# Kernel optimization log

Hardware: AMD Instinct MI355X
Metric: run time of the kernel (lower is better)

The kernel has to match this reference:

```python
import jax, jax.numpy as jnp
import numpy as np
from jax import lax

EPS = 1e-8

def _cosine_cost(x, y):
    # 1 - cosine_similarity over feature dim: [B,N,M]
    xn = x / jnp.clip(jnp.linalg.norm(x, axis=-1, keepdims=True), EPS)
    yn = y / jnp.clip(jnp.linalg.norm(y, axis=-1, keepdims=True), EPS)
    return 1.0 - jnp.einsum('bnd,bmd->bnm', xn, yn)

def _dtw_table(cost):
    # cost: [B,N,M] -> cumulative cost tc: [B,N,M]
    # tc[i,j] = cost[i,j] + min(tc[i-1,j-1], tc[i-1,j], tc[i,j-1])
    B, N, M = cost.shape
    row0 = jnp.cumsum(cost[:, 0, :], axis=1)  # [B,M]

    def col_step(left, inp):
        c, pdiag, pup = inp  # each [B]
        v = c + jnp.minimum(jnp.minimum(pdiag, pup), left)
        return v, v

    def row_step(prev, cost_row):
        # prev, cost_row: [B,M]
        first = prev[:, 0] + cost_row[:, 0]  # [B]
        xs = (cost_row[:, 1:].T, prev[:, :-1].T, prev[:, 1:].T)  # [M-1,B]
        _, rest = lax.scan(col_step, first, xs)  # [M-1,B]
        row = jnp.concatenate([first[:, None], rest.T], axis=1)  # [B,M]
        return row, row

    _, rows = lax.scan(row_step, row0, jnp.swapaxes(cost[:, 1:, :], 0, 1))
    tc = jnp.concatenate([row0[:, None, :], jnp.swapaxes(rows, 0, 1)], axis=1)
    return tc

def _backtrack(tc):
    # tc: [N,M] -> 0/1 path matrix [N,M]; tie-break diag > up > left,
    # matching the torch equality-chain order.
    N, M = tc.shape
    path0 = jnp.zeros((N, M), tc.dtype).at[N - 1, M - 1].set(1.0)

    def cond(s):
        i, j, _ = s
        return jnp.logical_and(i > 0, j > 0)

    def body(s):
        i, j, p = s
        a = tc[i - 1, j - 1]
        b = tc[i - 1, j]
        c = tc[i, j - 1]
        diag = jnp.logical_and(a <= b, a <= c)
        up = jnp.logical_and(jnp.logical_not(diag), b <= c)
        ni = jnp.where(jnp.logical_or(diag, up), i - 1, i)
        nj = jnp.where(jnp.logical_or(diag, jnp.logical_not(up)), j - 1, j)
        p = p.at[ni, nj].set(1.0)
        return ni, nj, p

    _, _, p = lax.while_loop(cond, body, (jnp.int32(N - 1), jnp.int32(M - 1), path0))
    return p.at[0, 0].set(1.0)

def setup_inputs() -> dict:
    key = jax.random.key(0)
    kx, ky = jax.random.split(key)
    B, N, M, D = 64, 512, 512, 256
    x = jax.random.normal(kx, (B, N, D), dtype=jnp.float32)
    y = jax.random.normal(ky, (B, M, D), dtype=jnp.float32)
    return {"x": x, "y": y}

def reference(x, y):
    cost = _cosine_cost(x, y)                 # [B,N,M]
    tc = _dtw_table(cost)                     # [B,N,M]
    path = jax.vmap(_backtrack)(tc)           # [B,N,M]
    pos = jax.nn.logsumexp(jnp.sum(cost * path, axis=1), axis=1)  # [B]
    neg = jax.nn.logsumexp(jnp.sum(cost, axis=1), axis=1)         # [B]
    return pos - neg
```

## Files before the change

kernel.cpp:

```cpp
#include <hip/hip_runtime.h>
#include <hip/hip_bf16.h>
#include <stdint.h>

typedef __attribute__((ext_vector_type(8))) short short8v;
typedef __attribute__((ext_vector_type(4))) float float4v;
typedef __attribute__((ext_vector_type(4))) unsigned short ushort4v;
typedef __attribute__((ext_vector_type(4))) unsigned int uint4v;

#define FINF __builtin_huge_valf()
#define BB 64
#define NN 512
#define DD 256
#define TT_SKEW 640


static __device__ __forceinline__ unsigned short f2bf(float f) {
  union { float f; uint32_t u; } a; a.f = f;
  uint32_t r = a.u + 0x7fffu + ((a.u >> 16) & 1u);
  return (unsigned short)(r >> 16);
}
static __device__ __forceinline__ float bf2f(uint16_t v) {
  return __uint_as_float(((uint32_t)v) << 16);
}

__global__ __launch_bounds__(64) void pad_zero_kernel(uint16_t* __restrict__ skew)
{
  const int tau = blockIdx.x, b = blockIdx.y, g = threadIdx.x;
  const int r = tau - 2 * g;
  if (r < 0 || r > 511) {
    uint16_t* p = skew + ((size_t)b * TT_SKEW + tau) * NN + g * 8;
    *(uint4v*)p = (uint4v){0u, 0u, 0u, 0u};
  }
}

__global__ __launch_bounds__(256) void norm_cast_kernel(
    const float* __restrict__ x, const float* __restrict__ y,
    uint16_t* __restrict__ xnb, uint16_t* __restrict__ ynb)
{
  const int wave = threadIdx.x >> 6, lane = threadIdx.x & 63;
  const int row = blockIdx.x * 4 + wave;
  const float* src; uint16_t* dst;
  if (row < BB * NN) { src = x + (size_t)row * DD;            dst = xnb + (size_t)row * DD; }
  else               { src = y + (size_t)(row - BB*NN) * DD;  dst = ynb + (size_t)(row - BB*NN) * DD; }
  const float4v v = *(const float4v*)(src + lane * 4);
  float s = v[0]*v[0] + v[1]*v[1] + v[2]*v[2] + v[3]*v[3];
  #pragma unroll
  for (int d = 1; d < 64; d <<= 1) s += __shfl_xor(s, d, 64);
  const float inv = 1.0f / fmaxf(sqrtf(s), 1e-8f);
  ushort4v o;
  o[0] = f2bf(v[0] * inv); o[1] = f2bf(v[1] * inv);
  o[2] = f2bf(v[2] * inv); o[3] = f2bf(v[3] * inv);
  *(ushort4v*)(dst + lane * 4) = o;
}

__global__ __launch_bounds__(256) void gemm_cost_kernel(
    const uint16_t* __restrict__ xnb, const uint16_t* __restrict__ ynb,
    uint16_t* __restrict__ skew)
{
  __shared__ uint16_t As[128 * 32];
  __shared__ uint16_t Bs[128 * 32];
  const int bid = blockIdx.x;
  const int b = bid >> 4, tm = (bid >> 2) & 3, tn = bid & 3;
  const int tid = threadIdx.x, wave = tid >> 6, lane = tid & 63;
  const int wr = wave >> 1, wc = wave & 1;

  const char* Ab = (const char*)(xnb + (size_t)b * NN * DD + (size_t)tm * 128 * DD);
  const char* Bb = (const char*)(ynb + (size_t)b * NN * DD + (size_t)tn * 128 * DD);

  float4v acc[4][4];
  #pragma unroll
  for (int i = 0; i < 4; i++)
    #pragma unroll
    for (int j = 0; j < 4; j++) acc[i][j] = (float4v){0.f, 0.f, 0.f, 0.f};

  const int seg0 = wave * 2;
  const int o0 = seg0 * 1024 + lane * 16;
  const int o1 = o0 + 1024;
  const int r0 = o0 >> 6, c0 = o0 & 63;
  const int r1 = o1 >> 6, c1 = o1 & 63;

  for (int kk = 0; kk < 8; kk++) {
    const int kb = kk * 64;
    __builtin_amdgcn_global_load_lds(
        (const __attribute__((address_space(1))) uint32_t*)(Ab + (size_t)r0 * 512 + kb + c0),
        (__attribute__((address_space(3))) uint32_t*)((char*)As + seg0 * 1024), 16, 0, 0);
    __builtin_amdgcn_global_load_lds(
        (const __attribute__((address_space(1))) uint32_t*)(Ab + (size_t)r1 * 512 + kb + c1),
        (__attribute__((address_space(3))) uint32_t*)((char*)As + (seg0 + 1) * 1024), 16, 0, 0);
    __builtin_amdgcn_global_load_lds(
        (const __attribute__((address_space(1))) uint32_t*)(Bb + (size_t)r0 * 512 + kb + c0),
        (__attribute__((address_space(3))) uint32_t*)((char*)Bs + seg0 * 1024), 16, 0, 0);
    __builtin_amdgcn_global_load_lds(
        (const __attribute__((address_space(1))) uint32_t*)(Bb + (size_t)r1 * 512 + kb + c1),
        (__attribute__((address_space(3))) uint32_t*)((char*)Bs + (seg0 + 1) * 1024), 16, 0, 0);
    __syncthreads();

    short8v af[4], bfr[4];
    #pragma unroll
    for (int mi = 0; mi < 4; mi++) {
      const int rr = wr * 64 + mi * 16 + (lane & 15);
      af[mi] = *(const short8v*)((const char*)As + rr * 64 + (lane >> 4) * 16);
    }
    #pragma unroll
    for (int nj = 0; nj < 4; nj++) {
      const int rr = wc * 64 + nj * 16 + (lane & 15);
      bfr[nj] = *(const short8v*)((const char*)Bs + rr * 64 + (lane >> 4) * 16);
    }
    #pragma unroll
    for (int mi = 0; mi < 4; mi++)
      #pragma unroll
      for (int nj = 0; nj < 4; nj++)
        acc[mi][nj] = __builtin_amdgcn_mfma_f32_16x16x32_bf16(af[mi], bfr[nj], acc[mi][nj], 0, 0, 0);
    __syncthreads();
  }

  uint16_t* Cb = skew + (size_t)b * TT_SKEW * NN;
  #pragma unroll
  for (int mi = 0; mi < 4; mi++)
    #pragma unroll
    for (int nj = 0; nj < 4; nj++) {
      const int cc = tn * 128 + wc * 64 + nj * 16 + (lane & 15);
      const int lg = cc >> 3;
      #pragma unroll
      for (int v = 0; v < 4; v++) {
        const int rr = tm * 128 + wr * 64 + mi * 16 + (lane >> 4) * 4 + v;
        Cb[(size_t)(rr + 2 * lg) * NN + cc] = f2bf(1.0f - acc[mi][nj][v]);
      }
    }
}

__global__ __launch_bounds__(256) void neg_lse_kernel(
    const uint16_t* __restrict__ skew, float* __restrict__ negbuf)
{
  __shared__ float sm[8];
  const int b = blockIdx.x, tid = threadIdx.x;
  const int wave = tid >> 6, lane = tid & 63;
  const uint32_t* p = (const uint32_t*)(skew + (size_t)b * TT_SKEW * NN) + tid;
  float s0 = 0.f, s1 = 0.f;
  #pragma unroll 8
  for (int t = 0; t < TT_SKEW; ++t) {
    const uint32_t w = p[t * 256];
    s0 += __uint_as_float(w << 16);
    s1 += __uint_as_float(w & 0xFFFF0000u);
  }
  float m = fmaxf(s0, s1);
  #pragma unroll
  for (int d = 1; d < 64; d <<= 1) m = fmaxf(m, __shfl_xor(m, d, 64));
  if (lane == 0) sm[wave] = m;
  __syncthreads();
  m = fmaxf(fmaxf(sm[0], sm[1]), fmaxf(sm[2], sm[3]));
  float e = expf(s0 - m) + expf(s1 - m);
  #pragma unroll
  for (int d = 1; d < 64; d <<= 1) e += __shfl_xor(e, d, 64);
  if (lane == 0) sm[4 + wave] = e;
  __syncthreads();
  if (tid == 0) negbuf[b] = m + logf(sm[4] + sm[5] + sm[6] + sm[7]);
}

__global__ __launch_bounds__(64, 1) void dtw_fwd_kernel(
    const uint16_t* __restrict__ skew, uint32_t* __restrict__ decg)
{
  extern __shared__ char lds_raw[];
  const int l = threadIdx.x;
  const int b = blockIdx.x;
  const uint16_t* csk = skew + (size_t)b * TT_SKEW * NN;
  const uint64_t base = (uint64_t)(uintptr_t)csk;
  const bool is0 = (l == 0);
  const uint32_t voff_base = 16u * (uint32_t)l;

  uint4v ringA[8], ringB[8];
  #pragma unroll
  for (int i = 0; i < 8; ++i) {
    const uint32_t voA = voff_base + ((uint32_t)(2 * i) << 10);
    const uint32_t voB = voA + 1024u;
    asm volatile("global_load_dwordx4 %0, %1, %2" : "=v"(ringA[i]) : "v"(voA), "s"(base));
    asm volatile("global_load_dwordx4 %0, %1, %2" : "=v"(ringB[i]) : "v"(voB), "s"(base));
  }

  float tp[8];
  #pragma unroll
  for (int c = 0; c < 8; ++c) tp[c] = FINF;
  float cl0 = FINF, cl1 = FINF, carry = FINF;
  const uint32_t dump_addr = 65536u + (((uint32_t)l) << 2);

  for (int t0 = 0; t0 < 320; t0 += 8) {
    #pragma unroll
    for (int u = 0; u < 8; ++u) {
      const int t = t0 + u;
      float shA = __shfl_up(cl0, 1, 64);
      float shB = __shfl_up(cl1, 1, 64);
      if (is0) { shA = (t == 0) ? 0.0f : FINF; shB = FINF; }
      const float sh_p0 = carry;
      carry = shB;

      asm volatile("s_waitcnt vmcnt(14)" : "+v"(ringA[u]), "+v"(ringB[u]));
      const uint4v A = ringA[u];
      const uint4v Bv = ringB[u];

      const uint32_t rlane = (uint32_t)(t - l);
      const bool valid = rlane < 256u;

      float ca[8], cbv[8], S0[8], S1[8];
      #pragma unroll
      for (int k = 0; k < 4; ++k) {
        ca[2*k]   = __uint_as_float(A[k] << 16);
        ca[2*k+1] = __uint_as_float(A[k] & 0xFFFF0000u);
        cbv[2*k]   = __uint_as_float(Bv[k] << 16);
        cbv[2*k+1] = __uint_as_float(Bv[k] & 0xFFFF0000u);
      }
      S0[0] = ca[0]; S1[0] = cbv[0];
      #pragma unroll
      for (int c = 1; c < 8; ++c) { S0[c] = S0[c-1] + ca[c]; S1[c] = S1[c-1] + cbv[c]; }

      float dcp0[8], mu0[8], w0[8], PW0[8], tn0[8];
      dcp0[0] = sh_p0;
      #pragma unroll
      for (int c = 1; c < 8; ++c) dcp0[c] = tp[c-1];
      #pragma unroll
      for (int c = 0; c < 8; ++c) mu0[c] = fminf(dcp0[c], tp[c]);
      w0[0] = mu0[0];
      #pragma unroll
      for (int c = 1; c < 8; ++c) w0[c] = mu0[c] - S0[c-1];
      PW0[0] = w0[0];
      #pragma unroll
      for (int c = 1; c < 8; ++c) PW0[c] = fminf(PW0[c-1], w0[c]);
      #pragma unroll
      for (int c = 0; c < 8; ++c) tn0[c] = fminf(PW0[c], shA) + S0[c];

      float dcp1[8], mu1[8], w1[8], PW1[8], tn1[8];
      dcp1[0] = shA;
      #pragma unroll
      for (int c = 1; c < 8; ++c) dcp1[c] = tn0[c-1];
      #pragma unroll
      for (int c = 0; c < 8; ++c) mu1[c] = fminf(dcp1[c], tn0[c]);
      w1[0] = mu1[0];
      #pragma unroll
      for (int c = 1; c < 8; ++c) w1[c] = mu1[c] - S1[c-1];
      PW1[0] = w1[0];
      #pragma unroll
      for (int c = 1; c < 8; ++c) PW1[c] = fminf(PW1[c-1], w1[c]);
      #pragma unroll
      for (int c = 0; c < 8; ++c) tn1[c] = fminf(PW1[c], shB) + S1[c];

      uint32_t word = 0;
      {
        float lc0[8], lc1[8];
        lc0[0] = shA; lc1[0] = shB;
        #pragma unroll
        for (int c = 1; c < 8; ++c) { lc0[c] = tn0[c-1]; lc1[c] = tn1[c-1]; }
        #pragma unroll
        for (int c = 0; c < 8; ++c) {
          const uint32_t e0 = (tp[c] < dcp0[c]) ? 1u : 0u;
          const uint32_t d0 = (lc0[c] < mu0[c]) ? 2u : e0;
          const uint32_t e1 = (tn0[c] < dcp1[c]) ? 1u : 0u;
          const uint32_t d1 = (lc1[c] < mu1[c]) ? 2u : e1;
          word |= (d0 << (2 * c)) | (d1 << (16 + 2 * c));
        }
      }
      const uint32_t waddr = valid ? ((rlane << 8) | (((uint32_t)l) << 2)) : dump_addr;
      *(uint32_t*)(lds_raw + waddr) = word;

      #pragma unroll
      for (int c = 0; c < 8; ++c) tp[c] = valid ? tn1[c] : tp[c];
      cl0 = valid ? tn0[7] : cl0;
      cl1 = tp[7];

      {
        int rr = 2 * (t + 8); if (rr > 638) rr = 638;
        const uint32_t voA = voff_base + ((uint32_t)rr << 10);
        const uint32_t voB = voA + 1024u;
        asm volatile("global_load_dwordx4 %0, %1, %2" : "=v"(ringA[u]) : "v"(voA), "s"(base));
        asm volatile("global_load_dwordx4 %0, %1, %2" : "=v"(ringB[u]) : "v"(voB), "s"(base));
      }
    }
  }
  asm volatile("s_waitcnt vmcnt(0)" ::: "memory");

  uint32_t* dg = decg + (size_t)b * 16384;
  #pragma unroll 4
  for (int i = 0; i < 64; ++i)
    *(uint4v*)(dg + i * 256 + l * 4) = *(const uint4v*)(lds_raw + i * 1024 + l * 16);
}

__global__ __launch_bounds__(64, 1) void dtw_bt_kernel(
    const uint16_t* __restrict__ skew, const uint32_t* __restrict__ decg,
    const float* __restrict__ negbuf, float* __restrict__ out)
{
  extern __shared__ char lds_raw[];
  uint16_t* rlo    = (uint16_t*)(lds_raw + 65536);
  uint16_t* rhi    = (uint16_t*)(lds_raw + 66560);
  float*    colpos = (float*)  (lds_raw + 67584);
  const uint32_t* dec32 = (const uint32_t*)lds_raw;

  const int l = threadIdx.x;
  const int b = blockIdx.x;
  const uint16_t* csk = skew + (size_t)b * TT_SKEW * NN;
  const uint32_t* dg = decg + (size_t)b * 16384;

  #pragma unroll 4
  for (int i = 0; i < 64; ++i)
    *(uint4v*)(lds_raw + i * 1024 + l * 16) = *(const uint4v*)(dg + i * 256 + l * 4);
  for (int r = l; r < NN; r += 64) { rlo[r] = 1; rhi[r] = 0; colpos[r] = 0.0f; }
  __syncthreads();

  if (l == 0) {
    int i = NN - 1, j = NN - 1, hicur = NN - 1;
    int cidx = -1; uint32_t cw = 0;
    while (i > 0 && j > 0) {
      const int widx = (i >> 1) * 64 + (j >> 3);
      if (widx != cidx) { cw = dec32[widx]; cidx = widx; }
      const uint32_t dd = (cw >> (((i & 1) << 4) + ((j & 7) << 1))) & 3u;
      if (dd == 2u) { j--; }
      else {
        rlo[i] = (uint16_t)j; rhi[i] = (uint16_t)hicur;
        i--;
        if (dd == 0u) j--;
        hicur = j;
      }
    }
    rlo[i] = (uint16_t)j; rhi[i] = (uint16_t)hicur;
  }
  __syncthreads();
  for (int r = l; r < NN; r += 64) {
    const int lo = rlo[r], hi = rhi[r];
    for (int j = lo; j <= hi; j++) {
      const float cv = bf2f(csk[(size_t)(r + 2 * (j >> 3)) * NN + j]);
      atomicAdd(&colpos[j], cv);
    }
  }
  if (l == 0 && rlo[0] != 0) atomicAdd(&colpos[0], bf2f(csk[0]));
  __syncthreads();

  float mv[8];
  float mx2 = -FINF;
  #pragma unroll
  for (int k = 0; k < 8; k++) { mv[k] = colpos[l + 64 * k]; mx2 = fmaxf(mx2, mv[k]); }
  #pragma unroll
  for (int d = 1; d < 64; d <<= 1) mx2 = fmaxf(mx2, __shfl_xor(mx2, d, 64));
  float se2 = 0.f;
  #pragma unroll
  for (int k = 0; k < 8; k++) se2 += expf(mv[k] - mx2);
  #pragma unroll
  for (int d = 1; d < 64; d <<= 1) se2 += __shfl_xor(se2, d, 64);
  const float pos = mx2 + logf(se2);

  if (l == 0) out[b] = pos - negbuf[b];
}

extern "C" void kernel_launch(void* const* d_in, const int* in_sizes, int n_in,
                              void* d_out, int out_size, void* d_ws, size_t ws_size,
                              hipStream_t stream)
{
  (void)in_sizes; (void)n_in; (void)out_size; (void)ws_size;
  const float* x = (const float*)d_in[0];
  const float* y = (const float*)d_in[1];
  float* out = (float*)d_out;
  char* ws = (char*)d_ws;
  uint16_t* xnb  = (uint16_t*)ws;
  uint16_t* ynb  = (uint16_t*)(ws + (size_t)16777216);
  uint16_t* skew = (uint16_t*)(ws + (size_t)33554432);
  float*  negbuf = (float*)  (ws + (size_t)75497472);
  uint32_t* decg = (uint32_t*)(ws + (size_t)75501568);

  (void)hipFuncSetAttribute((const void*)dtw_fwd_kernel,
                            hipFuncAttributeMaxDynamicSharedMemorySize, 65792);
  (void)hipFuncSetAttribute((const void*)dtw_bt_kernel,
                            hipFuncAttributeMaxDynamicSharedMemorySize, 69632);

  pad_zero_kernel<<<dim3(TT_SKEW, BB), 64, 0, stream>>>(skew);
  norm_cast_kernel<<<16384, 256, 0, stream>>>(x, y, xnb, ynb);
  gemm_cost_kernel<<<1024, 256, 0, stream>>>(xnb, ynb, skew);
  neg_lse_kernel<<<64, 256, 0, stream>>>(skew, negbuf);
  dtw_fwd_kernel<<<64, 64, 65792, stream>>>(skew, decg);
  dtw_bt_kernel<<<64, 64, 69632, stream>>>(skew, decg, negbuf, out);
}
```

Baseline: 297.9 us.

## Interleave two batches per wave in DTW forward and tile backtrack decision reads

Each forward DTW block now runs two independent batch recurrences back to back in the same loop. The aim is to hide shuffle, ALU and load latency of the serial wavefront with instruction-level parallelism. In exchange it launches half as many blocks, doubles LDS use, and shortens the prefetch ring from 8 to 4 steps. The backtrack loop now reads two decision words per 4x8 tile and walks inside the tile, which cuts reloads from LDS.

```diff
diff --git a/kernel.cpp b/kernel.cpp
--- a/kernel.cpp
+++ b/kernel.cpp
@@ -162,123 +162,132 @@
 {
   extern __shared__ char lds_raw[];
   const int l = threadIdx.x;
-  const int b = blockIdx.x;
-  const uint16_t* csk = skew + (size_t)b * TT_SKEW * NN;
-  const uint64_t base = (uint64_t)(uintptr_t)csk;
+  const int q = blockIdx.x;
+  const uint16_t* csk0 = skew + (size_t)(2 * q) * TT_SKEW * NN;
+  const uint16_t* csk1 = skew + (size_t)(2 * q + 1) * TT_SKEW * NN;
+  const uint64_t base0 = (uint64_t)(uintptr_t)csk0;
+  const uint64_t base1 = (uint64_t)(uintptr_t)csk1;
   const bool is0 = (l == 0);
   const uint32_t voff_base = 16u * (uint32_t)l;
-
-  uint4v ringA[8], ringB[8];
-  #pragma unroll
-  for (int i = 0; i < 8; ++i) {
+  const uint32_t dump_addr = 131072u + (((uint32_t)l) << 2);
+
+  uint4v rA0[4], rA1[4], rB0[4], rB1[4];
+  #pragma unroll
+  for (int i = 0; i < 4; ++i) {
     const uint32_t voA = voff_base + ((uint32_t)(2 * i) << 10);
     const uint32_t voB = voA + 1024u;
-    asm volatile("global_load_dwordx4 %0, %1, %2" : "=v"(ringA[i]) : "v"(voA), "s"(base));
-    asm volatile("global_load_dwordx4 %0, %1, %2" : "=v"(ringB[i]) : "v"(voB), "s"(base));
-  }
-
-  float tp[8];
-  #pragma unroll
-  for (int c = 0; c < 8; ++c) tp[c] = FINF;
-  float cl0 = FINF, cl1 = FINF, carry = FINF;
-  const uint32_t dump_addr = 65536u + (((uint32_t)l) << 2);
-
-  for (int t0 = 0; t0 < 320; t0 += 8) {
-    #pragma unroll
-    for (int u = 0; u < 8; ++u) {
+    asm volatile("global_load_dwordx4 %0, %1, %2" : "=v"(rA0[i]) : "v"(voA), "s"(base0));
+    asm volatile("global_load_dwordx4 %0, %1, %2" : "=v"(rA1[i]) : "v"(voB), "s"(base0));
+    asm volatile("global_load_dwordx4 %0, %1, %2" : "=v"(rB0[i]) : "v"(voA), "s"(base1));
+    asm volatile("global_load_dwordx4 %0, %1, %2" : "=v"(rB1[i]) : "v"(voB), "s"(base1));
+  }
+
+  float tpA[8], tpB[8];
+  #pragma unroll
+  for (int c = 0; c < 8; ++c) { tpA[c] = FINF; tpB[c] = FINF; }
+  float clA0 = FINF, clA1 = FINF, carA = FINF;
+  float clB0 = FINF, clB1 = FINF, carB = FINF;
+
+  auto STEP = [&](int t, uint32_t rlane, bool valid,
+                  const uint4v A, const uint4v Bv,
+                  float (&tp)[8], float &cl0, float &cl1, float &carry,
+                  uint32_t dec_off) {
+    float shA = __shfl_up(cl0, 1, 64);
+    float shB = __shfl_up(cl1, 1, 64);
+    if (is0) { shA = (t == 0) ? 0.0f : FINF; shB = FINF; }
+    const float sh_p0 = carry;
+    carry = shB;
+
+    float ca[8], cbv[8], S0[8], S1[8];
+    #pragma unroll
+    for (int k = 0; k < 4; ++k) {
+      ca[2*k]    = __uint_as_float(A[k] << 16);
+      ca[2*k+1]  = __uint_as_float(A[k] & 0xFFFF0000u);
+      cbv[2*k]   = __uint_as_float(Bv[k] << 16);
+      cbv[2*k+1] = __uint_as_float(Bv[k] & 0xFFFF0000u);
+    }
+    S0[0] = ca[0]; S1[0] = cbv[0];
+    #pragma unroll
+    for (int c = 1; c < 8; ++c) { S0[c] = S0[c-1] + ca[c]; S1[c] = S1[c-1] + cbv[c]; }
+
+    float dcp0[8], mu0[8], w0[8], PW0[8], tn0[8];
+    dcp0[0] = sh_p0;
+    #pragma unroll
+    for (int c = 1; c < 8; ++c) dcp0[c] = tp[c-1];
+    #pragma unroll
+    for (int c = 0; c < 8; ++c) mu0[c] = fminf(dcp0[c], tp[c]);
+    w0[0] = mu0[0];
+    #pragma unroll
+    for (int c = 1; c < 8; ++c) w0[c] = mu0[c] - S0[c-1];
+    PW0[0] = w0[0];
+    #pragma unroll
+    for (int c = 1; c < 8; ++c) PW0[c] = fminf(PW0[c-1], w0[c]);
+    #pragma unroll
+    for (int c = 0; c < 8; ++c) tn0[c] = fminf(PW0[c], shA) + S0[c];
+
+    float dcp1[8], mu1[8], w1[8], PW1[8], tn1[8];
+    dcp1[0] = shA;
+    #pragma unroll
+    for (int c = 1; c < 8; ++c) dcp1[c] = tn0[c-1];
+    #pragma unroll
+    for (int c = 0; c < 8; ++c) mu1[c] = fminf(dcp1[c], tn0[c]);
+    w1[0] = mu1[0];
+    #pragma unroll
+    for (int c = 1; c < 8; ++c) w1[c] = mu1[c] - S1[c-1];
+    PW1[0] = w1[0];
+    #pragma unroll
+    for (int c = 1; c < 8; ++c) PW1[c] = fminf(PW1[c-1], w1[c]);
+    #pragma unroll
+    for (int c = 0; c < 8; ++c) tn1[c] = fminf(PW1[c], shB) + S1[c];
+
+    uint32_t word = 0;
+    {
+      float lc0[8], lc1[8];
+      lc0[0] = shA; lc1[0] = shB;
+      #pragma unroll
+      for (int c = 1; c < 8; ++c) { lc0[c] = tn0[c-1]; lc1[c] = tn1[c-1]; }
+      #pragma unroll
+      for (int c = 0; c < 8; ++c) {
+        const uint32_t e0 = (tp[c] < dcp0[c]) ? 1u : 0u;
+        const uint32_t d0 = (lc0[c] < mu0[c]) ? 2u : e0;
+        const uint32_t e1 = (tn0[c] < dcp1[c]) ? 1u : 0u;
+        const uint32_t d1 = (lc1[c] < mu1[c]) ? 2u : e1;
+        word |= (d0 << (2 * c)) | (d1 << (16 + 2 * c));
+      }
+    }
+    const uint32_t waddr = valid ? (dec_off + (rlane << 8) + (((uint32_t)l) << 2)) : dump_addr;
+    *(uint32_t*)(lds_raw + waddr) = word;
+
+    #pragma unroll
+    for (int c = 0; c < 8; ++c) tp[c] = valid ? tn1[c] : tp[c];
+    cl0 = valid ? tn0[7] : cl0;
+    cl1 = tp[7];
+  };
+
+  for (int t0 = 0; t0 < 320; t0 += 4) {
+    #pragma unroll
+    for (int u = 0; u < 4; ++u) {
       const int t = t0 + u;
-      float shA = __shfl_up(cl0, 1, 64);
-      float shB = __shfl_up(cl1, 1, 64);
-      if (is0) { shA = (t == 0) ? 0.0f : FINF; shB = FINF; }
-      const float sh_p0 = carry;
-      carry = shB;
-
-      asm volatile("s_waitcnt vmcnt(14)" : "+v"(ringA[u]), "+v"(ringB[u]));
-      const uint4v A = ringA[u];
-      const uint4v Bv = ringB[u];
-
+      asm volatile("s_waitcnt vmcnt(12)"
+                   : "+v"(rA0[u]), "+v"(rA1[u]), "+v"(rB0[u]), "+v"(rB1[u]));
       const uint32_t rlane = (uint32_t)(t - l);
       const bool valid = rlane < 256u;
-
-      float ca[8], cbv[8], S0[8], S1[8];
-      #pragma unroll
-      for (int k = 0; k < 4; ++k) {
-        ca[2*k]   = __uint_as_float(A[k] << 16);
-        ca[2*k+1] = __uint_as_float(A[k] & 0xFFFF0000u);
-        cbv[2*k]   = __uint_as_float(Bv[k] << 16);
-        cbv[2*k+1] = __uint_as_float(Bv[k] & 0xFFFF0000u);
-      }
-      S0[0] = ca[0]; S1[0] = cbv[0];
-      #pragma unroll
-      for (int c = 1; c < 8; ++c) { S0[c] = S0[c-1] + ca[c]; S1[c] = S1[c-1] + cbv[c]; }
-
-      float dcp0[8], mu0[8], w0[8], PW0[8], tn0[8];
-      dcp0[0] = sh_p0;
-      #pragma unroll
-      for (int c = 1; c < 8; ++c) dcp0[c] = tp[c-1];
-      #pragma unroll
-      for (int c = 0; c < 8; ++c) mu0[c] = fminf(dcp0[c], tp[c]);
-      w0[0] = mu0[0];
-      #pragma unroll
-      for (int c = 1; c < 8; ++c) w0[c] = mu0[c] - S0[c-1];
-      PW0[0] = w0[0];
-      #pragma unroll
-      for (int c = 1; c < 8; ++c) PW0[c] = fminf(PW0[c-1], w0[c]);
-      #pragma unroll
-      for (int c = 0; c < 8; ++c) tn0[c] = fminf(PW0[c], shA) + S0[c];
-
-      float dcp1[8], mu1[8], w1[8], PW1[8], tn1[8];
-      dcp1[0] = shA;
-      #pragma unroll
-      for (int c = 1; c < 8; ++c) dcp1[c] = tn0[c-1];
-      #pragma unroll
-      for (int c = 0; c < 8; ++c) mu1[c] = fminf(dcp1[c], tn0[c]);
-      w1[0] = mu1[0];
-      #pragma unroll
-      for (int c = 1; c < 8; ++c) w1[c] = mu1[c] - S1[c-1];
-      PW1[0] = w1[0];
-      #pragma unroll
-      for (int c = 1; c < 8; ++c) PW1[c] = fminf(PW1[c-1], w1[c]);
-      #pragma unroll
-      for (int c = 0; c < 8; ++c) tn1[c] = fminf(PW1[c], shB) + S1[c];
-
-      uint32_t word = 0;
-      {
-        float lc0[8], lc1[8];
-        lc0[0] = shA; lc1[0] = shB;
-        #pragma unroll
-        for (int c = 1; c < 8; ++c) { lc0[c] = tn0[c-1]; lc1[c] = tn1[c-1]; }
-        #pragma unroll
-        for (int c = 0; c < 8; ++c) {
-          const uint32_t e0 = (tp[c] < dcp0[c]) ? 1u : 0u;
-          const uint32_t d0 = (lc0[c] < mu0[c]) ? 2u : e0;
-          const uint32_t e1 = (tn0[c] < dcp1[c]) ? 1u : 0u;
-          const uint32_t d1 = (lc1[c] < mu1[c]) ? 2u : e1;
-          word |= (d0 << (2 * c)) | (d1 << (16 + 2 * c));
-        }
-      }
-      const uint32_t waddr = valid ? ((rlane << 8) | (((uint32_t)l) << 2)) : dump_addr;
-      *(uint32_t*)(lds_raw + waddr) = word;
-
-      #pragma unroll
-      for (int c = 0; c < 8; ++c) tp[c] = valid ? tn1[c] : tp[c];
-      cl0 = valid ? tn0[7] : cl0;
-      cl1 = tp[7];
-
-      {
-        int rr = 2 * (t + 8); if (rr > 638) rr = 638;
-        const uint32_t voA = voff_base + ((uint32_t)rr << 10);
-        const uint32_t voB = voA + 1024u;
-        asm volatile("global_load_dwordx4 %0, %1, %2" : "=v"(ringA[u]) : "v"(voA), "s"(base));
-        asm volatile("global_load_dwordx4 %0, %1, %2" : "=v"(ringB[u]) : "v"(voB), "s"(base));
-      }
+      STEP(t, rlane, valid, rA0[u], rA1[u], tpA, clA0, clA1, carA, 0u);
+      STEP(t, rlane, valid, rB0[u], rB1[u], tpB, clB0, clB1, carB, 65536u);
+      int rr = 2 * (t + 4); if (rr > 638) rr = 638;
+      const uint32_t voA = voff_base + ((uint32_t)rr << 10);
+      const uint32_t voB = voA + 1024u;
+      asm volatile("global_load_dwordx4 %0, %1, %2" : "=v"(rA0[u]) : "v"(voA), "s"(base0));
+      asm volatile("global_load_dwordx4 %0, %1, %2" : "=v"(rA1[u]) : "v"(voB), "s"(base0));
+      asm volatile("global_load_dwordx4 %0, %1, %2" : "=v"(rB0[u]) : "v"(voA), "s"(base1));
+      asm volatile("global_load_dwordx4 %0, %1, %2" : "=v"(rB1[u]) : "v"(voB), "s"(base1));
     }
   }
   asm volatile("s_waitcnt vmcnt(0)" ::: "memory");
 
-  uint32_t* dg = decg + (size_t)b * 16384;
+  uint32_t* dg = decg + (size_t)q * 32768;
   #pragma unroll 4
-  for (int i = 0; i < 64; ++i)
+  for (int i = 0; i < 128; ++i)
     *(uint4v*)(dg + i * 256 + l * 4) = *(const uint4v*)(lds_raw + i * 1024 + l * 16);
 }
 
@@ -305,17 +314,20 @@
 
   if (l == 0) {
     int i = NN - 1, j = NN - 1, hicur = NN - 1;
-    int cidx = -1; uint32_t cw = 0;
     while (i > 0 && j > 0) {
-      const int widx = (i >> 1) * 64 + (j >> 3);
-      if (widx != cidx) { cw = dec32[widx]; cidx = widx; }
-      const uint32_t dd = (cw >> (((i & 1) << 4) + ((j & 7) << 1))) & 3u;
-      if (dd == 2u) { j--; }
-      else {
-        rlo[i] = (uint16_t)j; rhi[i] = (uint16_t)hicur;
-        i--;
-        if (dd == 0u) j--;
-        hicur = j;
+      const int a = i >> 2, g = j >> 3;
+      const uint32_t w0 = dec32[a * 128 + g];
+      const uint32_t w1 = dec32[a * 128 + 64 + g];
+      while (i > 0 && j > 0 && (i >> 2) == a && (j >> 3) == g) {
+        const uint32_t w = (i & 2) ? w1 : w0;
+        const uint32_t dd = (w >> (((i & 1) << 4) + ((j & 7) << 1))) & 3u;
+        if (dd == 2u) { j--; }
+        else {
+          rlo[i] = (uint16_t)j; rhi[i] = (uint16_t)hicur;
+          i--;
+          if (dd == 0u) j--;
+          hicur = j;
+        }
       }
     }
     rlo[i] = (uint16_t)j; rhi[i] = (uint16_t)hicur;
@@ -363,7 +375,7 @@
   uint32_t* decg = (uint32_t*)(ws + (size_t)75501568);
 
   (void)hipFuncSetAttribute((const void*)dtw_fwd_kernel,
-                            hipFuncAttributeMaxDynamicSharedMemorySize, 65792);
+                            hipFuncAttributeMaxDynamicSharedMemorySize, 131584);
   (void)hipFuncSetAttribute((const void*)dtw_bt_kernel,
                             hipFuncAttributeMaxDynamicSharedMemorySize, 69632);
 
@@ -371,6 +383,6 @@
   norm_cast_kernel<<<16384, 256, 0, stream>>>(x, y, xnb, ynb);
   gemm_cost_kernel<<<1024, 256, 0, stream>>>(xnb, ynb, skew);
   neg_lse_kernel<<<64, 256, 0, stream>>>(skew, negbuf);
-  dtw_fwd_kernel<<<64, 64, 65792, stream>>>(skew, decg);
+  dtw_fwd_kernel<<<32, 64, 131584, stream>>>(skew, decg);
   dtw_bt_kernel<<<64, 64, 69632, stream>>>(skew, decg, negbuf, out);
 }
```

New measurement: 412.6 us. 1.39x slower.

## Fuse neg-LSE into GEMM epilogue and merge DTW forward with backtrack

Applied to the files above, without the earlier changes.

Per-column cost sums are now accumulated with atomics in the GEMM epilogue, which removes the separate neg_lse kernel that re-read the whole skewed cost buffer. The DTW forward and backtrack kernels are merged so the decision bits stay in LDS instead of going to global memory and back. The pad-zeroing kernel is dropped; a small lane-0 boundary fix replaces its role. The padded regions of the skew buffer are now left uninitialised, which is a correctness risk if any computation reads them. Float atomics also make the column sums order-dependent.

```diff
diff --git a/kernel.cpp b/kernel.cpp
--- a/kernel.cpp
+++ b/kernel.cpp
@@ -23,14 +23,9 @@
   return __uint_as_float(((uint32_t)v) << 16);
 }
 
-__global__ __launch_bounds__(64) void pad_zero_kernel(uint16_t* __restrict__ skew)
-{
-  const int tau = blockIdx.x, b = blockIdx.y, g = threadIdx.x;
-  const int r = tau - 2 * g;
-  if (r < 0 || r > 511) {
-    uint16_t* p = skew + ((size_t)b * TT_SKEW + tau) * NN + g * 8;
-    *(uint4v*)p = (uint4v){0u, 0u, 0u, 0u};
-  }
+__global__ __launch_bounds__(256) void zero_colsum_kernel(float* __restrict__ colsum)
+{
+  colsum[blockIdx.x * 256 + threadIdx.x] = 0.0f;
 }
 
 __global__ __launch_bounds__(256) void norm_cast_kernel(
@@ -55,7 +50,7 @@
 
 __global__ __launch_bounds__(256) void gemm_cost_kernel(
     const uint16_t* __restrict__ xnb, const uint16_t* __restrict__ ynb,
-    uint16_t* __restrict__ skew)
+    uint16_t* __restrict__ skew, float* __restrict__ colsum)
 {
   __shared__ uint16_t As[128 * 32];
   __shared__ uint16_t Bs[128 * 32];
@@ -127,38 +122,24 @@
         Cb[(size_t)(rr + 2 * lg) * NN + cc] = f2bf(1.0f - acc[mi][nj][v]);
       }
     }
-}
-
-__global__ __launch_bounds__(256) void neg_lse_kernel(
-    const uint16_t* __restrict__ skew, float* __restrict__ negbuf)
-{
-  __shared__ float sm[8];
-  const int b = blockIdx.x, tid = threadIdx.x;
-  const int wave = tid >> 6, lane = tid & 63;
-  const uint32_t* p = (const uint32_t*)(skew + (size_t)b * TT_SKEW * NN) + tid;
-  float s0 = 0.f, s1 = 0.f;
-  #pragma unroll 8
-  for (int t = 0; t < TT_SKEW; ++t) {
-    const uint32_t w = p[t * 256];
-    s0 += __uint_as_float(w << 16);
-    s1 += __uint_as_float(w & 0xFFFF0000u);
-  }
-  float m = fmaxf(s0, s1);
-  #pragma unroll
-  for (int d = 1; d < 64; d <<= 1) m = fmaxf(m, __shfl_xor(m, d, 64));
-  if (lane == 0) sm[wave] = m;
-  __syncthreads();
-  m = fmaxf(fmaxf(sm[0], sm[1]), fmaxf(sm[2], sm[3]));
-  float e = expf(s0 - m) + expf(s1 - m);
-  #pragma unroll
-  for (int d = 1; d < 64; d <<= 1) e += __shfl_xor(e, d, 64);
-  if (lane == 0) sm[4 + wave] = e;
-  __syncthreads();
-  if (tid == 0) negbuf[b] = m + logf(sm[4] + sm[5] + sm[6] + sm[7]);
-}
-
-__global__ __launch_bounds__(64, 1) void dtw_fwd_kernel(
-    const uint16_t* __restrict__ skew, uint32_t* __restrict__ decg)
+
+  #pragma unroll
+  for (int nj = 0; nj < 4; nj++) {
+    const int cc = tn * 128 + wc * 64 + nj * 16 + (lane & 15);
+    float s = 0.f;
+    #pragma unroll
+    for (int mi = 0; mi < 4; mi++)
+      #pragma unroll
+      for (int v = 0; v < 4; v++) s += 1.0f - acc[mi][nj][v];
+    s += __shfl_xor(s, 16, 64);
+    s += __shfl_xor(s, 32, 64);
+    if (lane < 16) atomicAdd(&colsum[b * 512 + cc], s);
+  }
+}
+
+__global__ __launch_bounds__(64, 1) void dtw_fwdbt_kernel(
+    const uint16_t* __restrict__ skew, const float* __restrict__ colsum,
+    float* __restrict__ out)
 {
   extern __shared__ char lds_raw[];
   const int l = threadIdx.x;
@@ -167,6 +148,7 @@
   const uint64_t base = (uint64_t)(uintptr_t)csk;
   const bool is0 = (l == 0);
   const uint32_t voff_base = 16u * (uint32_t)l;
+  const uint32_t dump_addr = 65536u + (((uint32_t)l) << 2);
 
   uint4v ringA[8], ringB[8];
   #pragma unroll
@@ -181,7 +163,6 @@
   #pragma unroll
   for (int c = 0; c < 8; ++c) tp[c] = FINF;
   float cl0 = FINF, cl1 = FINF, carry = FINF;
-  const uint32_t dump_addr = 65536u + (((uint32_t)l) << 2);
 
   for (int t0 = 0; t0 < 320; t0 += 8) {
     #pragma unroll
@@ -192,6 +173,7 @@
       if (is0) { shA = (t == 0) ? 0.0f : FINF; shB = FINF; }
       const float sh_p0 = carry;
       carry = shB;
+      const float shA1 = is0 ? FINF : shA;
 
       asm volatile("s_waitcnt vmcnt(14)" : "+v"(ringA[u]), "+v"(ringB[u]));
       const uint4v A = ringA[u];
@@ -228,7 +210,7 @@
       for (int c = 0; c < 8; ++c) tn0[c] = fminf(PW0[c], shA) + S0[c];
 
       float dcp1[8], mu1[8], w1[8], PW1[8], tn1[8];
-      dcp1[0] = shA;
+      dcp1[0] = shA1;
       #pragma unroll
       for (int c = 1; c < 8; ++c) dcp1[c] = tn0[c-1];
       #pragma unroll
@@ -257,7 +239,7 @@
           word |= (d0 << (2 * c)) | (d1 << (16 + 2 * c));
         }
       }
-      const uint32_t waddr = valid ? ((rlane << 8) | (((uint32_t)l) << 2)) : dump_addr;
+      const uint32_t waddr = valid ? ((rlane << 8) + (((uint32_t)l) << 2)) : dump_addr;
       *(uint32_t*)(lds_raw + waddr) = word;
 
       #pragma unroll
@@ -275,32 +257,28 @@
     }
   }
   asm volatile("s_waitcnt vmcnt(0)" ::: "memory");
-
-  uint32_t* dg = decg + (size_t)b * 16384;
-  #pragma unroll 4
-  for (int i = 0; i < 64; ++i)
-    *(uint4v*)(dg + i * 256 + l * 4) = *(const uint4v*)(lds_raw + i * 1024 + l * 16);
-}
-
-__global__ __launch_bounds__(64, 1) void dtw_bt_kernel(
-    const uint16_t* __restrict__ skew, const uint32_t* __restrict__ decg,
-    const float* __restrict__ negbuf, float* __restrict__ out)
-{
-  extern __shared__ char lds_raw[];
-  uint16_t* rlo    = (uint16_t*)(lds_raw + 65536);
-  uint16_t* rhi    = (uint16_t*)(lds_raw + 66560);
-  float*    colpos = (float*)  (lds_raw + 67584);
+  __syncthreads();
+
+  uint16_t* rlo    = (uint16_t*)(lds_raw + 65792);
+  uint16_t* rhi    = (uint16_t*)(lds_raw + 66816);
+  float*    colpos = (float*)  (lds_raw + 67840);
   const uint32_t* dec32 = (const uint32_t*)lds_raw;
 
-  const int l = threadIdx.x;
-  const int b = blockIdx.x;
-  const uint16_t* csk = skew + (size_t)b * TT_SKEW * NN;
-  const uint32_t* dg = decg + (size_t)b * 16384;
-
-  #pragma unroll 4
-  for (int i = 0; i < 64; ++i)
-    *(uint4v*)(lds_raw + i * 1024 + l * 16) = *(const uint4v*)(dg + i * 256 + l * 4);
   for (int r = l; r < NN; r += 64) { rlo[r] = 1; rhi[r] = 0; colpos[r] = 0.0f; }
+
+  const float* cs = colsum + (size_t)b * 512;
+  float nv[8];
+  float m = -FINF;
+  #pragma unroll
+  for (int k = 0; k < 8; ++k) { nv[k] = cs[l + 64 * k]; m = fmaxf(m, nv[k]); }
+  #pragma unroll
+  for (int d = 1; d < 64; d <<= 1) m = fmaxf(m, __shfl_xor(m, d, 64));
+  float e = 0.f;
+  #pragma unroll
+  for (int k = 0; k < 8; ++k) e += expf(nv[k] - m);
+  #pragma unroll
+  for (int d = 1; d < 64; d <<= 1) e += __shfl_xor(e, d, 64);
+  const float neg = m + logf(e);
   __syncthreads();
 
   if (l == 0) {
@@ -321,6 +299,7 @@
     rlo[i] = (uint16_t)j; rhi[i] = (uint16_t)hicur;
   }
   __syncthreads();
+
   for (int r = l; r < NN; r += 64) {
     const int lo = rlo[r], hi = rhi[r];
     for (int j = lo; j <= hi; j++) {
@@ -344,7 +323,7 @@
   for (int d = 1; d < 64; d <<= 1) se2 += __shfl_xor(se2, d, 64);
   const float pos = mx2 + logf(se2);
 
-  if (l == 0) out[b] = pos - negbuf[b];
+  if (l == 0) out[b] = pos - neg;
 }
 
 extern "C" void kernel_launch(void* const* d_in, const int* in_sizes, int n_in,
@@ -356,21 +335,16 @@
   const float* y = (const float*)d_in[1];
   float* out = (float*)d_out;
   char* ws = (char*)d_ws;
-  uint16_t* xnb  = (uint16_t*)ws;
-  uint16_t* ynb  = (uint16_t*)(ws + (size_t)16777216);
-  uint16_t* skew = (uint16_t*)(ws + (size_t)33554432);
-  float*  negbuf = (float*)  (ws + (size_t)75497472);
-  uint32_t* decg = (uint32_t*)(ws + (size_t)75501568);
-
-  (void)hipFuncSetAttribute((const void*)dtw_fwd_kernel,
-                            hipFuncAttributeMaxDynamicSharedMemorySize, 65792);
-  (void)hipFuncSetAttribute((const void*)dtw_bt_kernel,
-                            hipFuncAttributeMaxDynamicSharedMemorySize, 69632);
-
-  pad_zero_kernel<<<dim3(TT_SKEW, BB), 64, 0, stream>>>(skew);
+  uint16_t* xnb   = (uint16_t*)ws;
+  uint16_t* ynb   = (uint16_t*)(ws + (size_t)16777216);
+  uint16_t* skew  = (uint16_t*)(ws + (size_t)33554432);
+  float*   colsum = (float*)   (ws + (size_t)75497472);
+
+  (void)hipFuncSetAttribute((const void*)dtw_fwdbt_kernel,
+                            hipFuncAttributeMaxDynamicSharedMemorySize, 69888);
+
+  zero_colsum_kernel<<<128, 256, 0, stream>>>(colsum);
   norm_cast_kernel<<<16384, 256, 0, stream>>>(x, y, xnb, ynb);
-  gemm_cost_kernel<<<1024, 256, 0, stream>>>(xnb, ynb, skew);
-  neg_lse_kernel<<<64, 256, 0, stream>>>(skew, negbuf);
-  dtw_fwd_kernel<<<64, 64, 65792, stream>>>(skew, decg);
-  dtw_bt_kernel<<<64, 64, 69632, stream>>>(skew, decg, negbuf, out);
-}
+  gemm_cost_kernel<<<1024, 256, 0, stream>>>(xnb, ynb, skew, colsum);
+  dtw_fwdbt_kernel<<<64, 64, 69888, stream>>>(skew, colsum, out);
+}
```

Result: faster. 251.7 us (median of 2 runs) (-15.5%).
